# Kernel optimization log

Hardware: AMD Instinct MI355X
Metric: run time of the kernel (lower is better)

The kernel has to match this reference:

```python
import jax, jax.numpy as jnp
import numpy as np

N = 8192
IN_F = 512
OUT_F = 256
NEG_INF = -9e15
SCORE_DIV = 8.0


def setup_inputs() -> dict:
    key = jax.random.key(0)
    k1, k2, k3, k4 = jax.random.split(key, 4)
    x = jax.random.normal(k1, (N, IN_F), dtype=jnp.float32)
    adj = jax.random.randint(k2, (N, N), 0, 2, dtype=jnp.int32)
    # Xavier-uniform-like params (gain 1.414), as in the torch module
    limW = 1.414 * np.sqrt(6.0 / (IN_F + OUT_F))
    W = jax.random.uniform(k3, (IN_F, OUT_F), dtype=jnp.float32, minval=-limW, maxval=limW)
    lima = 1.414 * np.sqrt(6.0 / (OUT_F + 1))
    a = jax.random.uniform(k4, (OUT_F, 1), dtype=jnp.float32, minval=-lima, maxval=lima)
    return {"input": x, "adj": adj, "W": W, "a": a}


def reference(input, adj, W, a):
    # h: [N, F]
    h = input @ W
    # e[i, j] = sum_k h[i,k] * h[j,k] * a[k]  (equivalent to the repeat/cat/mul path)
    e = (h * a[:, 0]) @ h.T  # [N, N]
    e = jnp.where(adj > 0, e, jnp.float32(NEG_INF))
    attention = jax.nn.softmax(e / SCORE_DIV, axis=1)  # dropout is identity in eval
    h_prime = attention @ h  # [N, F]
    return jax.nn.elu(h_prime)
```

## Files before the change

### kernel.cpp

```cpp
#include <hip/hip_runtime.h>

#define N_ 8192
#define INF_ 512
#define OUTF_ 256
#define KVSPLIT 8
#define BK 32
#define BQ 128
#define NTILES (N_ / KVSPLIT / BK)

typedef float f32x4 __attribute__((ext_vector_type(4)));
typedef float f32x16 __attribute__((ext_vector_type(16)));
typedef __bf16 bf16x8 __attribute__((ext_vector_type(8)));

__device__ __forceinline__ unsigned short f2bf(float f) {
  union { float f; unsigned u; } v; v.f = f;
  unsigned r = v.u + 0x7fffu + ((v.u >> 16) & 1u);
  return (unsigned short)(r >> 16);
}
__device__ __forceinline__ float bf2f(unsigned short u) {
  union { unsigned u; float f; } v; v.u = ((unsigned)u) << 16;
  return v.f;
}

__global__ __launch_bounds__(256) void k_prep(
    const float* __restrict__ x, const float* __restrict__ W,
    unsigned short* __restrict__ xhi, unsigned short* __restrict__ xlo,
    unsigned short* __restrict__ WT)
{
  int idx = blockIdx.x * 256 + threadIdx.x;
  float4 v = ((const float4*)x)[idx];
  float f[4] = {v.x, v.y, v.z, v.w};
  unsigned short h[4], lo[4];
#pragma unroll
  for (int j = 0; j < 4; ++j) {
    h[j] = f2bf(f[j]);
    lo[j] = f2bf(f[j] - bf2f(h[j]));
  }
  *(uint2*)&xhi[idx * 4] = *(uint2*)h;
  *(uint2*)&xlo[idx * 4] = *(uint2*)lo;
  if (idx < INF_ * OUTF_) {
    int c = idx & (OUTF_ - 1);
    int k = idx >> 8;
    WT[c * INF_ + k] = f2bf(W[k * OUTF_ + c]);
  }
}

__global__ __launch_bounds__(256) void k_gemm_h(
    const unsigned short* __restrict__ xhi, const unsigned short* __restrict__ xlo,
    const unsigned short* __restrict__ WT,
    unsigned short* __restrict__ hK, unsigned short* __restrict__ hT)
{
  const int tid = threadIdx.x;
  const int w = tid >> 6, l = tid & 63, g = l >> 4, li = l & 15;
  const int r0 = blockIdx.x * 64 + w * 16;
  const int c0 = blockIdx.y * 64;

  f32x4 acc[4];
  const f32x4 z4 = {0.f, 0.f, 0.f, 0.f};
#pragma unroll
  for (int n = 0; n < 4; ++n) acc[n] = z4;

  const unsigned short* xh = xhi + (size_t)(r0 + li) * INF_ + g * 8;
  const unsigned short* xl = xlo + (size_t)(r0 + li) * INF_ + g * 8;
  const unsigned short* wt = WT + (size_t)(c0 + li) * INF_ + g * 8;

#pragma unroll 4
  for (int kc = 0; kc < 16; ++kc) {
    bf16x8 Ah = *(const bf16x8*)(xh + kc * 32);
    bf16x8 Al = *(const bf16x8*)(xl + kc * 32);
#pragma unroll
    for (int n = 0; n < 4; ++n) {
      bf16x8 Bn = *(const bf16x8*)(wt + (size_t)n * 16 * INF_ + kc * 32);
      acc[n] = __builtin_amdgcn_mfma_f32_16x16x32_bf16(Ah, Bn, acc[n], 0, 0, 0);
      acc[n] = __builtin_amdgcn_mfma_f32_16x16x32_bf16(Al, Bn, acc[n], 0, 0, 0);
    }
  }
#pragma unroll
  for (int n = 0; n < 4; ++n)
#pragma unroll
    for (int s = 0; s < 4; ++s) {
      unsigned short b = f2bf(acc[n][s]);
      int row = r0 + 4 * g + s;
      int col = c0 + n * 16 + li;
      hK[(size_t)row * OUTF_ + col] = b;
      hT[(size_t)col * N_ + row] = b;
    }
}

__global__ __launch_bounds__(256, 2) void k_attn(
    const unsigned short* __restrict__ hK, const unsigned short* __restrict__ hT,
    const int* __restrict__ adj, const float* __restrict__ a,
    unsigned short* __restrict__ Opart, float* __restrict__ lsum)
{
  __shared__ __align__(16) unsigned char smem[65536];
  unsigned char* KA = smem;
  unsigned char* VA = smem + 16384;
  unsigned char* KB = smem + 32768;
  unsigned char* VB = smem + 49152;

  const int tid = threadIdx.x;
  const int w = tid >> 6, l = tid & 63;
  const int q32 = l & 31;
  const int hi = l >> 5;
  const int bid = blockIdx.x;
  const int split = bid & 7;
  const int qblk = (bid >> 3) * BQ;
  const int qrw = qblk + w * 32;
  const int jb = split * (N_ / KVSPLIT);
  const float SCALE = 0.18033688011112042f;

  int offK[4], offV[4];
#pragma unroll
  for (int p = 0; p < 4; ++p) {
    int ch = tid + p * 256;
    int rK = ch >> 5, cK = ch & 31;
    offK[p] = rK * OUTF_ + ((cK ^ (rK & 7)) * 8);
    int dV = ch >> 2, cV = ch & 3;
    offV[p] = dV * N_ + ((cV ^ ((dV ^ (dV >> 2)) & 3)) * 8);
  }
  const int kbase = q32 * 512;
  const int ehk = (hi ^ (q32 & 7)) << 4;
  const int sv = (q32 ^ (q32 >> 2)) & 3;
  const int c0v = (sv & 2) | (hi ^ (sv & 1));
  const int voff0 = q32 * 64 + (c0v << 4);

  const int* adjp = adj + (size_t)(qrw + q32) * N_ + jb + 4 * hi;

  bf16x8 Qf[16];
  {
    const unsigned short* hp = hK + (size_t)(qrw + q32) * OUTF_;
#pragma unroll
    for (int kt = 0; kt < 16; ++kt) {
      const int off = kt * 16 + 8 * hi;
      bf16x8 hv = *(const bf16x8*)(hp + off);
      float4 a0 = *(const float4*)(a + off);
      float4 a1 = *(const float4*)(a + off + 4);
      bf16x8 q;
      q[0] = (__bf16)((float)hv[0] * (a0.x * SCALE));
      q[1] = (__bf16)((float)hv[1] * (a0.y * SCALE));
      q[2] = (__bf16)((float)hv[2] * (a0.z * SCALE));
      q[3] = (__bf16)((float)hv[3] * (a0.w * SCALE));
      q[4] = (__bf16)((float)hv[4] * (a1.x * SCALE));
      q[5] = (__bf16)((float)hv[5] * (a1.y * SCALE));
      q[6] = (__bf16)((float)hv[6] * (a1.z * SCALE));
      q[7] = (__bf16)((float)hv[7] * (a1.w * SCALE));
      Qf[kt] = q;
    }
  }

  f32x16 O[8];
#pragma unroll
  for (int dt = 0; dt < 8; ++dt)
#pragma unroll
    for (int r = 0; r < 16; ++r) O[dt][r] = 0.f;
  float lp2[2] = {0.f, 0.f};

#define STAGE(tt, Kd, Vd) do { \
    const unsigned short* _hk = hK + (size_t)(jb + (tt) * BK) * OUTF_; \
    const unsigned short* _ht = hT + (jb + (tt) * BK); \
    _Pragma("unroll") \
    for (int p = 0; p < 4; ++p) \
      __builtin_amdgcn_global_load_lds( \
        (const __attribute__((address_space(1))) void*)(_hk + offK[p]), \
        (__attribute__((address_space(3))) void*)((Kd) + (p * 256 + w * 64) * 16), 16, 0, 0); \
    _Pragma("unroll") \
    for (int p = 0; p < 4; ++p) \
      __builtin_amdgcn_global_load_lds( \
        (const __attribute__((address_space(1))) void*)(_ht + offV[p]), \
        (__attribute__((address_space(3))) void*)((Vd) + (p * 256 + w * 64) * 16), 16, 0, 0); \
    __builtin_amdgcn_sched_barrier(0);  \
  } while (0)

#define PIPEBAR() do { \
    __builtin_amdgcn_sched_barrier(0); \
    asm volatile("s_waitcnt vmcnt(2)" ::: "memory"); \
    __builtin_amdgcn_sched_barrier(0); \
    __builtin_amdgcn_s_barrier(); \
    __builtin_amdgcn_sched_barrier(0); \
  } while (0)

  int4 ad[4];
  STAGE(0, KA, VA);
#pragma unroll
  for (int i = 0; i < 4; ++i) ad[i] = *(const int4*)(adjp + i * 8);
  __syncthreads();

#pragma unroll 1
  for (int t = 0; t < NTILES; ++t) {
    const unsigned char* Kc = (t & 1) ? KB : KA;
    const unsigned char* Vc = (t & 1) ? VB : VA;
    unsigned char* Kn = (t & 1) ? KA : KB;
    unsigned char* Vn = (t & 1) ? VA : VB;
    if (t < NTILES - 1) STAGE(t + 1, Kn, Vn);

    f32x16 St;
#pragma unroll
    for (int r = 0; r < 16; ++r) St[r] = 0.f;
    __builtin_amdgcn_s_setprio(1);
#pragma unroll
    for (int kt = 0; kt < 16; ++kt) {
      bf16x8 kf = *(const bf16x8*)(Kc + kbase + ((kt << 5) ^ ehk));
      St = __builtin_amdgcn_mfma_f32_32x32x16_bf16(kf, Qf[kt], St, 0, 0, 0);
    }
    __builtin_amdgcn_s_setprio(0);

    unsigned pk[8];
#pragma unroll
    for (int i = 0; i < 8; ++i) {
      int m0, m1;
      const int4 av = ad[i >> 1];
      if ((i & 1) == 0) { m0 = av.x; m1 = av.y; }
      else             { m0 = av.z; m1 = av.w; }
      float e0 = exp2f(St[2 * i]);
      float e1 = exp2f(St[2 * i + 1]);
      float v0 = m0 ? e0 : 0.f;
      float v1 = m1 ? e1 : 0.f;
      lp2[i & 1] += v0 + v1;
      asm("v_cvt_pk_bf16_f32 %0, %1, %2" : "=v"(pk[i]) : "v"(v0), "v"(v1));
    }

    if (t + 1 < NTILES) {
#pragma unroll
      for (int i = 0; i < 4; ++i) ad[i] = *(const int4*)(adjp + (t + 1) * 32 + i * 8);
    }

    bf16x8 Pf[2];
#pragma unroll
    for (int tt = 0; tt < 2; ++tt) {
      unsigned u0 = pk[4 * tt],     u2 = pk[4 * tt + 2];
      unsigned u1 = pk[4 * tt + 1], u3 = pk[4 * tt + 3];
      asm("v_permlane32_swap_b32 %0, %1" : "+v"(u0), "+v"(u2));
      asm("v_permlane32_swap_b32 %0, %1" : "+v"(u1), "+v"(u3));
      union { unsigned u[4]; bf16x8 v; } pu;
      pu.u[0] = u0; pu.u[1] = u1; pu.u[2] = u2; pu.u[3] = u3;
      Pf[tt] = pu.v;
    }

    __builtin_amdgcn_s_setprio(1);
#pragma unroll
    for (int dt = 0; dt < 8; ++dt) {
      bf16x8 v0 = *(const bf16x8*)(Vc + dt * 2048 + voff0);
      bf16x8 v1 = *(const bf16x8*)(Vc + dt * 2048 + (voff0 ^ 32));
      O[dt] = __builtin_amdgcn_mfma_f32_32x32x16_bf16(Pf[0], v0, O[dt], 0, 0, 0);
      O[dt] = __builtin_amdgcn_mfma_f32_32x32x16_bf16(Pf[1], v1, O[dt], 0, 0, 0);
    }
    __builtin_amdgcn_s_setprio(0);

    PIPEBAR();
  }
#undef STAGE
#undef PIPEBAR

  {
    float lpv = lp2[0] + lp2[1];
    float lfull = lpv + __shfl_xor(lpv, 32);
    if (l < 32)
      lsum[(size_t)split * N_ + qrw + q32] = lfull;
  }
  const size_t ob = (size_t)split * N_ * OUTF_;
#pragma unroll
  for (int dt = 0; dt < 8; ++dt)
#pragma unroll
    for (int r = 0; r < 16; ++r) {
      int q = (r & 3) + 8 * (r >> 2) + 4 * hi;
      Opart[ob + (size_t)(qrw + q) * OUTF_ + dt * 32 + q32] = f2bf(O[dt][r]);
    }
}

__global__ __launch_bounds__(256) void k_combine(
    const unsigned short* __restrict__ Opart, const float* __restrict__ lsum,
    float* __restrict__ out)
{
  int idx = blockIdx.x * 256 + threadIdx.x;
  int row = idx >> 6;
  int c = (idx & 63) * 4;
  float L = 0.f, a0 = 0.f, a1 = 0.f, a2 = 0.f, a3 = 0.f;
#pragma unroll
  for (int s = 0; s < KVSPLIT; ++s) {
    L += lsum[(size_t)s * N_ + row];
    uint2 o = *(const uint2*)(Opart + ((size_t)s * N_ + row) * OUTF_ + c);
    a0 += bf2f((unsigned short)(o.x & 0xffff));
    a1 += bf2f((unsigned short)(o.x >> 16));
    a2 += bf2f((unsigned short)(o.y & 0xffff));
    a3 += bf2f((unsigned short)(o.y >> 16));
  }
  float inv = 1.f / L;
  float r0 = a0 * inv, r1 = a1 * inv, r2 = a2 * inv, r3 = a3 * inv;
  float4 r;
  r.x = r0 > 0.f ? r0 : expm1f(r0);
  r.y = r1 > 0.f ? r1 : expm1f(r1);
  r.z = r2 > 0.f ? r2 : expm1f(r2);
  r.w = r3 > 0.f ? r3 : expm1f(r3);
  *(float4*)(out + (size_t)row * OUTF_ + c) = r;
}

extern "C" void kernel_launch(void* const* d_in, const int* in_sizes, int n_in,
                              void* d_out, int out_size, void* d_ws, size_t ws_size,
                              hipStream_t stream) {
  const float* x  = (const float*)d_in[0];
  const int* adj  = (const int*)d_in[1];
  const float* W  = (const float*)d_in[2];
  const float* a  = (const float*)d_in[3];
  float* out = (float*)d_out;
  char* ws = (char*)d_ws;

  unsigned short* hK = (unsigned short*)(ws);
  unsigned short* hT = (unsigned short*)(ws + (size_t)4 * 1024 * 1024);
  unsigned short* WT = (unsigned short*)(ws + (size_t)8 * 1024 * 1024);
  float* lsum = (float*)(ws + (size_t)9 * 1024 * 1024);
  unsigned short* Opart = (unsigned short*)(ws + (size_t)10 * 1024 * 1024);
  unsigned short* xhi = (unsigned short*)(ws + (size_t)10 * 1024 * 1024);
  unsigned short* xlo = (unsigned short*)(ws + (size_t)18 * 1024 * 1024);

  k_prep<<<(N_ * INF_ / 4) / 256, 256, 0, stream>>>(x, W, xhi, xlo, WT);
  dim3 g1(N_ / 64, OUTF_ / 64);
  k_gemm_h<<<g1, 256, 0, stream>>>(xhi, xlo, WT, hK, hT);
  k_attn<<<(N_ / BQ) * KVSPLIT, 256, 0, stream>>>(hK, hT, adj, a, Opart, lsum);
  k_combine<<<(N_ * 64) / 256, 256, 0, stream>>>(Opart, lsum, out);
}
```

Before: 159.6 us.

## Software-pipeline QK of next tile with PV of current tile

Restructures the attention main loop so that K is staged two tiles ahead and V one tile ahead. The QK^T MFMAs for tile t+1 are interleaved with the PV MFMAs for tile t, with a prologue and epilogue added. The aim is to keep the matrix units busy while softmax and the exp/permlane work happen, and to hide load latency. In exchange it raises register pressure (St, Pf and pk live across iterations) and replaces the fine-grained vmcnt barrier with full __syncthreads.

```diff
diff --git a/kernel.cpp b/kernel.cpp
--- a/kernel.cpp
+++ b/kernel.cpp
@@ -155,101 +155,130 @@
     for (int r = 0; r < 16; ++r) O[dt][r] = 0.f;
   float lp2[2] = {0.f, 0.f};
 
-#define STAGE(tt, Kd, Vd) do { \
+#define STAGEK(tt, Kd) do { \
     const unsigned short* _hk = hK + (size_t)(jb + (tt) * BK) * OUTF_; \
-    const unsigned short* _ht = hT + (jb + (tt) * BK); \
     _Pragma("unroll") \
     for (int p = 0; p < 4; ++p) \
       __builtin_amdgcn_global_load_lds( \
         (const __attribute__((address_space(1))) void*)(_hk + offK[p]), \
         (__attribute__((address_space(3))) void*)((Kd) + (p * 256 + w * 64) * 16), 16, 0, 0); \
+  } while (0)
+#define STAGEV(tt, Vd) do { \
+    const unsigned short* _ht = hT + (jb + (tt) * BK); \
     _Pragma("unroll") \
     for (int p = 0; p < 4; ++p) \
       __builtin_amdgcn_global_load_lds( \
         (const __attribute__((address_space(1))) void*)(_ht + offV[p]), \
         (__attribute__((address_space(3))) void*)((Vd) + (p * 256 + w * 64) * 16), 16, 0, 0); \
-    __builtin_amdgcn_sched_barrier(0);  \
   } while (0)
 
-#define PIPEBAR() do { \
-    __builtin_amdgcn_sched_barrier(0); \
-    asm volatile("s_waitcnt vmcnt(2)" ::: "memory"); \
-    __builtin_amdgcn_sched_barrier(0); \
-    __builtin_amdgcn_s_barrier(); \
-    __builtin_amdgcn_sched_barrier(0); \
+#define SOFTMAX() do { \
+    _Pragma("unroll") \
+    for (int i = 0; i < 8; ++i) { \
+      int m0, m1; \
+      const int4 av = ad[i >> 1]; \
+      if ((i & 1) == 0) { m0 = av.x; m1 = av.y; } \
+      else             { m0 = av.z; m1 = av.w; } \
+      float e0 = exp2f(St[2 * i]); \
+      float e1 = exp2f(St[2 * i + 1]); \
+      float v0 = m0 ? e0 : 0.f; \
+      float v1 = m1 ? e1 : 0.f; \
+      lp2[i & 1] += v0 + v1; \
+      asm("v_cvt_pk_bf16_f32 %0, %1, %2" : "=v"(pk[i]) : "v"(v0), "v"(v1)); \
+    } \
   } while (0)
 
+#define MKPF() do { \
+    _Pragma("unroll") \
+    for (int tt = 0; tt < 2; ++tt) { \
+      unsigned u0 = pk[4 * tt],     u2 = pk[4 * tt + 2]; \
+      unsigned u1 = pk[4 * tt + 1], u3 = pk[4 * tt + 3]; \
+      asm("v_permlane32_swap_b32 %0, %1" : "+v"(u0), "+v"(u2)); \
+      asm("v_permlane32_swap_b32 %0, %1" : "+v"(u1), "+v"(u3)); \
+      union { unsigned u[4]; bf16x8 v; } pu; \
+      pu.u[0] = u0; pu.u[1] = u1; pu.u[2] = u2; pu.u[3] = u3; \
+      Pf[tt] = pu.v; \
+    } \
+  } while (0)
+
   int4 ad[4];
-  STAGE(0, KA, VA);
+  unsigned pk[8];
+  bf16x8 Pf[2];
+  f32x16 St;
+
+  STAGEK(0, KA);
+  STAGEV(0, VA);
 #pragma unroll
   for (int i = 0; i < 4; ++i) ad[i] = *(const int4*)(adjp + i * 8);
   __syncthreads();
+  STAGEK(1, KB);
+  {
+#pragma unroll
+    for (int r = 0; r < 16; ++r) St[r] = 0.f;
+    const unsigned char* kb = KA + kbase;
+#pragma unroll
+    for (int kt = 0; kt < 16; ++kt) {
+      bf16x8 kf = *(const bf16x8*)(kb + ((kt << 5) ^ ehk));
+      St = __builtin_amdgcn_mfma_f32_32x32x16_bf16(kf, Qf[kt], St, 0, 0, 0);
+    }
+    SOFTMAX();
+  }
+  __syncthreads();
 
 #pragma unroll 1
-  for (int t = 0; t < NTILES; ++t) {
-    const unsigned char* Kc = (t & 1) ? KB : KA;
-    const unsigned char* Vc = (t & 1) ? VB : VA;
-    unsigned char* Kn = (t & 1) ? KA : KB;
-    unsigned char* Vn = (t & 1) ? VA : VB;
-    if (t < NTILES - 1) STAGE(t + 1, Kn, Vn);
-
-    f32x16 St;
+  for (int t = 0; t < NTILES - 1; ++t) {
+    unsigned char* Kstage = (t & 1) ? KB : KA;
+    const unsigned char* Knext = (t & 1) ? KA : KB;
+    unsigned char* Vstage = (t & 1) ? VA : VB;
+    const unsigned char* Vcur  = (t & 1) ? VB : VA;
+
+    if (t + 2 < NTILES) STAGEK(t + 2, Kstage);
+    STAGEV(t + 1, Vstage);
+#pragma unroll
+    for (int i = 0; i < 4; ++i) ad[i] = *(const int4*)(adjp + (t + 1) * 32 + i * 8);
+
+    MKPF();
+
 #pragma unroll
     for (int r = 0; r < 16; ++r) St[r] = 0.f;
+    {
+      const unsigned char* kb = Knext + kbase;
+      __builtin_amdgcn_s_setprio(1);
+#pragma unroll
+      for (int s = 0; s < 8; ++s) {
+        bf16x8 kf0 = *(const bf16x8*)(kb + (((2 * s) << 5) ^ ehk));
+        bf16x8 kf1 = *(const bf16x8*)(kb + (((2 * s + 1) << 5) ^ ehk));
+        bf16x8 v0  = *(const bf16x8*)(Vcur + s * 2048 + voff0);
+        bf16x8 v1  = *(const bf16x8*)(Vcur + s * 2048 + (voff0 ^ 32));
+        St   = __builtin_amdgcn_mfma_f32_32x32x16_bf16(kf0, Qf[2 * s], St, 0, 0, 0);
+        O[s] = __builtin_amdgcn_mfma_f32_32x32x16_bf16(Pf[0], v0, O[s], 0, 0, 0);
+        St   = __builtin_amdgcn_mfma_f32_32x32x16_bf16(kf1, Qf[2 * s + 1], St, 0, 0, 0);
+        O[s] = __builtin_amdgcn_mfma_f32_32x32x16_bf16(Pf[1], v1, O[s], 0, 0, 0);
+      }
+      __builtin_amdgcn_s_setprio(0);
+    }
+    SOFTMAX();
+
+    __syncthreads();
+  }
+
+  MKPF();
+  {
+    const unsigned char* Vlast = ((NTILES - 1) & 1) ? VB : VA;
     __builtin_amdgcn_s_setprio(1);
 #pragma unroll
-    for (int kt = 0; kt < 16; ++kt) {
-      bf16x8 kf = *(const bf16x8*)(Kc + kbase + ((kt << 5) ^ ehk));
-      St = __builtin_amdgcn_mfma_f32_32x32x16_bf16(kf, Qf[kt], St, 0, 0, 0);
+    for (int s = 0; s < 8; ++s) {
+      bf16x8 v0 = *(const bf16x8*)(Vlast + s * 2048 + voff0);
+      bf16x8 v1 = *(const bf16x8*)(Vlast + s * 2048 + (voff0 ^ 32));
+      O[s] = __builtin_amdgcn_mfma_f32_32x32x16_bf16(Pf[0], v0, O[s], 0, 0, 0);
+      O[s] = __builtin_amdgcn_mfma_f32_32x32x16_bf16(Pf[1], v1, O[s], 0, 0, 0);
     }
     __builtin_amdgcn_s_setprio(0);
-
-    unsigned pk[8];
-#pragma unroll
-    for (int i = 0; i < 8; ++i) {
-      int m0, m1;
-      const int4 av = ad[i >> 1];
-      if ((i & 1) == 0) { m0 = av.x; m1 = av.y; }
-      else             { m0 = av.z; m1 = av.w; }
-      float e0 = exp2f(St[2 * i]);
-      float e1 = exp2f(St[2 * i + 1]);
-      float v0 = m0 ? e0 : 0.f;
-      float v1 = m1 ? e1 : 0.f;
-      lp2[i & 1] += v0 + v1;
-      asm("v_cvt_pk_bf16_f32 %0, %1, %2" : "=v"(pk[i]) : "v"(v0), "v"(v1));
-    }
-
-    if (t + 1 < NTILES) {
-#pragma unroll
-      for (int i = 0; i < 4; ++i) ad[i] = *(const int4*)(adjp + (t + 1) * 32 + i * 8);
-    }
-
-    bf16x8 Pf[2];
-#pragma unroll
-    for (int tt = 0; tt < 2; ++tt) {
-      unsigned u0 = pk[4 * tt],     u2 = pk[4 * tt + 2];
-      unsigned u1 = pk[4 * tt + 1], u3 = pk[4 * tt + 3];
-      asm("v_permlane32_swap_b32 %0, %1" : "+v"(u0), "+v"(u2));
-      asm("v_permlane32_swap_b32 %0, %1" : "+v"(u1), "+v"(u3));
-      union { unsigned u[4]; bf16x8 v; } pu;
-      pu.u[0] = u0; pu.u[1] = u1; pu.u[2] = u2; pu.u[3] = u3;
-      Pf[tt] = pu.v;
-    }
-
-    __builtin_amdgcn_s_setprio(1);
-#pragma unroll
-    for (int dt = 0; dt < 8; ++dt) {
-      bf16x8 v0 = *(const bf16x8*)(Vc + dt * 2048 + voff0);
-      bf16x8 v1 = *(const bf16x8*)(Vc + dt * 2048 + (voff0 ^ 32));
-      O[dt] = __builtin_amdgcn_mfma_f32_32x32x16_bf16(Pf[0], v0, O[dt], 0, 0, 0);
-      O[dt] = __builtin_amdgcn_mfma_f32_32x32x16_bf16(Pf[1], v1, O[dt], 0, 0, 0);
-    }
-    __builtin_amdgcn_s_setprio(0);
-
-    PIPEBAR();
-  }
-#undef STAGE
-#undef PIPEBAR
+  }
+#undef STAGEK
+#undef STAGEV
+#undef SOFTMAX
+#undef MKPF
 
   {
     float lpv = lp2[0] + lp2[1];
```

Result: faster. 153.4 us (-3.9%).
